# Kernel tuning notes

Measured on AMD Instinct MI355X. Metric: run time of the kernel, lower is better.

Reference implementation:

```python
import jax, jax.numpy as jnp
import numpy as np

K = 4  # number of conv kernel experts in CondConv_down


def setup_inputs() -> dict:
    key = jax.random.key(0)
    ks = jax.random.split(key, 8)
    N, Cin, H, W = 8, 64, 384, 384
    Cin2, Cout4, Cout2 = Cin // 2, 128 // 4, 128 // 2  # 32, 32, 64
    return {
        "x": jax.random.normal(ks[0], (N, Cin, H, W), jnp.float32),
        # square conv: Conv2d(in=64, out=64, 3x3, stride 2, pad 1, bias)
        "sq_w": jax.random.normal(ks[1], (Cout2, Cin, 3, 3), jnp.float32) * 0.05,
        "sq_b": jnp.zeros((Cout2,), jnp.float32),
        # vertical CondConv: attention 1x1 conv (== linear on pooled feats) + K expert kernels [3,1]
        "att_w_v": jax.random.normal(ks[2], (K, Cin2), jnp.float32) * 0.1,
        "att_b_v": jnp.zeros((K,), jnp.float32),
        "w_v": jax.random.normal(ks[3], (K, Cout4, Cin2, 3, 1), jnp.float32) * 0.05,
        "bn_v_g": jnp.ones((Cout4,), jnp.float32),
        "bn_v_b": jnp.zeros((Cout4,), jnp.float32),
        # horizontal CondConv: K expert kernels [1,3]
        "att_w_h": jax.random.normal(ks[4], (K, Cin2), jnp.float32) * 0.1,
        "att_b_h": jnp.zeros((K,), jnp.float32),
        "w_h": jax.random.normal(ks[5], (K, Cout4, Cin2, 1, 3), jnp.float32) * 0.05,
        "bn_h_g": jnp.ones((Cout4,), jnp.float32),
        "bn_h_b": jnp.zeros((Cout4,), jnp.float32),
    }


def _condconv(x, att_w, att_b, w, pad):
    # Attention: global avg pool -> 1x1 conv -> sigmoid (note: sigmoid, not softmax, as in source)
    att = jax.nn.sigmoid(jnp.mean(x, axis=(2, 3)) @ att_w.T + att_b)  # [N, K]
    # Aggregate expert kernels per sample: [N, Cout, Cin, kh, kw]
    agg = jnp.einsum("nk,koihw->noihw", att, w)
    def one(xi, wi):
        return jax.lax.conv_general_dilated(
            xi[None], wi, window_strides=(2, 2),
            padding=[(pad[0], pad[0]), (pad[1], pad[1])],
            dimension_numbers=("NCHW", "OIHW", "NCHW"))[0]
    return jax.vmap(one)(x, agg)  # per-sample dynamic conv == groups=N grouped conv


def _bn(x, g, b, eps=1e-5):
    # training-mode BatchNorm2d: batch statistics over (N, H, W), biased variance
    m = jnp.mean(x, axis=(0, 2, 3), keepdims=True)
    v = jnp.var(x, axis=(0, 2, 3), keepdims=True)
    return (x - m) * jax.lax.rsqrt(v + eps) * g[None, :, None, None] + b[None, :, None, None]


def _shuffle(x, g=8):
    N, C, H, W = x.shape
    return x.reshape(N, g, C // g, H, W).transpose(0, 2, 1, 3, 4).reshape(N, C, H, W)


def reference(x, sq_w, sq_b, att_w_v, att_b_v, w_v, bn_v_g, bn_v_b,
              att_w_h, att_b_h, w_h, bn_h_g, bn_h_b):
    sq = jax.lax.conv_general_dilated(
        x, sq_w, window_strides=(2, 2), padding=[(1, 1), (1, 1)],
        dimension_numbers=("NCHW", "OIHW", "NCHW")) + sq_b[None, :, None, None]
    x1, x2 = jnp.split(x, 2, axis=1)
    v = _bn(_condconv(x1, att_w_v, att_b_v, w_v, (1, 0)), bn_v_g, bn_v_b)
    h = _bn(_condconv(x2, att_w_h, att_b_h, w_h, (0, 1)), bn_h_g, bn_h_b)
    out = jnp.concatenate([sq, v, h], axis=1)  # [N, 128, H/2, W/2]
    return _shuffle(out, 8)
```

## Files before the change

kernel.cpp:

```cpp
#include <hip/hip_runtime.h>

#define NB    8
#define HIN   384
#define WIN   384
#define HOUT  192
#define WOUT  192
#define HW_IN (HIN * WIN)
#define PLANE (HOUT * WOUT)
#define CNT_BN (NB * HOUT * WOUT)

#define WS_MEANS 0
#define WS_AGGV  512
#define WS_AGGH  25088
#define WS_SQW   49664
#define WS_STATS 86528
#define WS_BN    86656

__global__ void k_zero(float* __restrict__ ws) {
    for (int i = threadIdx.x; i < 512; i += 256) ws[WS_MEANS + i] = 0.f;
    if (threadIdx.x < 128) ws[WS_STATS + threadIdx.x] = 0.f;
}

__global__ __launch_bounds__(256) void k_means(const float* __restrict__ x,
                                               float* __restrict__ ws) {
    int bc = blockIdx.x;
    int part = blockIdx.y;
    const float4* p = (const float4*)(x + (size_t)bc * HW_IN) + part * (HW_IN / 16);
    float s = 0.f;
    for (int i = threadIdx.x; i < HW_IN / 16; i += 256) {
        float4 v = p[i];
        s += (v.x + v.y) + (v.z + v.w);
    }
    __shared__ float red[256];
    red[threadIdx.x] = s;
    __syncthreads();
    for (int off = 128; off > 0; off >>= 1) {
        if ((int)threadIdx.x < off) red[threadIdx.x] += red[threadIdx.x + off];
        __syncthreads();
    }
    if (threadIdx.x == 0) atomicAdd(&ws[WS_MEANS + bc], red[0]);
}

__global__ void k_agg(const float* __restrict__ aw_v, const float* __restrict__ ab_v,
                      const float* __restrict__ wv,
                      const float* __restrict__ aw_h, const float* __restrict__ ab_h,
                      const float* __restrict__ wh, float* __restrict__ ws) {
    int n = blockIdx.x;
    __shared__ float att[8];
    if (threadIdx.x < 8) {
        int k = threadIdx.x & 3;
        int hsel = threadIdx.x >> 2;
        const float* m = ws + WS_MEANS + n * 64 + hsel * 32;
        const float* aw = hsel ? aw_h : aw_v;
        const float* ab = hsel ? ab_h : ab_v;
        float dot = 0.f;
        for (int c = 0; c < 32; c++) dot += m[c] * aw[k * 32 + c];
        float z = ab[k] + dot * (1.0f / HW_IN);
        att[threadIdx.x] = 1.0f / (1.0f + expf(-z));
    }
    __syncthreads();
    for (int i = threadIdx.x; i < 3072; i += 256) {
        int o = i & 31;
        int r = i >> 5;
        float sv = 0.f, sh = 0.f;
#pragma unroll
        for (int k = 0; k < 4; k++) {
            sv += att[k]     * wv[(k * 32 + o) * 96 + r];
            sh += att[4 + k] * wh[(k * 32 + o) * 96 + r];
        }
        ws[WS_AGGV + n * 3072 + i] = sv;
        ws[WS_AGGH + n * 3072 + i] = sh;
    }
}

__global__ void k_cvtw(const float* __restrict__ sq_w, float* __restrict__ ws) {
    int i = blockIdx.x * 256 + threadIdx.x;
    int oc = i & 63;
    int r = i >> 6;
    int c = r / 9, q = r % 9;
    ws[WS_SQW + i] = sq_w[(oc * 64 + c) * 9 + q];
}

__global__ __launch_bounds__(192) void k_sq(const float* __restrict__ x,
                                            const float* __restrict__ sq_b,
                                            const float* __restrict__ ws,
                                            float* __restrict__ out) {
    int xo = threadIdx.x;
    int yo = blockIdx.x;
    int n  = blockIdx.y;
    const float* wp = ws + WS_SQW;
    float acc[64];
#pragma unroll
    for (int j = 0; j < 64; j++) acc[j] = sq_b[j];
    const float* xb = x + (size_t)n * 64 * HW_IN;
    int c2 = 2 * xo;
    int iy0 = 2 * yo - 1;
    for (int c = 0; c < 64; c++) {
        const float* xc = xb + (size_t)c * HW_IN;
        float v[9];
#pragma unroll
        for (int ky = 0; ky < 3; ky++) {
            int iy = iy0 + ky;
            if (iy >= 0) {
                const float* row = xc + (size_t)iy * WIN;
                float2 v12 = *(const float2*)(row + c2);
                v[ky * 3 + 0] = (xo > 0) ? row[c2 - 1] : 0.f;
                v[ky * 3 + 1] = v12.x;
                v[ky * 3 + 2] = v12.y;
            } else {
                v[ky * 3 + 0] = v[ky * 3 + 1] = v[ky * 3 + 2] = 0.f;
            }
        }
        const float* wc = wp + c * 576;
#pragma unroll
        for (int t = 0; t < 9; t++) {
            float vv = v[t];
#pragma unroll
            for (int j = 0; j < 64; j++) acc[j] += vv * wc[t * 64 + j];
        }
    }
    size_t ob = (size_t)n * 128 * PLANE + (size_t)yo * WOUT + xo;
#pragma unroll
    for (int j = 0; j < 64; j++) {
        int co = ((j & 15) << 3) | (j >> 4);
        out[ob + (size_t)co * PLANE] = acc[j];
    }
}

__global__ __launch_bounds__(192) void k_vh(const float* __restrict__ x,
                                            const float* __restrict__ ws,
                                            float* __restrict__ out) {
    int xo = threadIdx.x, yo = blockIdx.x, n = blockIdx.y;
    int horz = blockIdx.z;
    float acc[32];
#pragma unroll
    for (int j = 0; j < 32; j++) acc[j] = 0.f;
    if (!horz) {
        const float* wn = ws + WS_AGGV + n * 3072;
        const float* xb = x + (size_t)n * 64 * HW_IN;
        int c2 = 2 * xo;
        int iy0 = 2 * yo - 1;
#pragma unroll 4
        for (int c = 0; c < 32; c++) {
            const float* xc = xb + (size_t)c * HW_IN;
            float v[3];
#pragma unroll
            for (int t = 0; t < 3; t++) {
                int iy = iy0 + t;
                v[t] = (iy >= 0) ? xc[(size_t)iy * WIN + c2] : 0.f;
            }
#pragma unroll
            for (int t = 0; t < 3; t++) {
                const float* wr = wn + (c * 3 + t) * 32;
#pragma unroll
                for (int j = 0; j < 32; j++) acc[j] += v[t] * wr[j];
            }
        }
    } else {
        const float* wn = ws + WS_AGGH + n * 3072;
        const float* xb = x + ((size_t)n * 64 + 32) * HW_IN;
        int c2 = 2 * xo;
#pragma unroll 4
        for (int c = 0; c < 32; c++) {
            const float* row = xb + (size_t)c * HW_IN + (size_t)(2 * yo) * WIN;
            float2 v12 = *(const float2*)(row + c2);
            float v0 = (xo > 0) ? row[c2 - 1] : 0.f;
            const float* wr = wn + c * 96;
#pragma unroll
            for (int j = 0; j < 32; j++)
                acc[j] += v0 * wr[j] + v12.x * wr[32 + j] + v12.y * wr[64 + j];
        }
    }
    int cb = horz ? 96 : 64;
    size_t ob = (size_t)n * 128 * PLANE + (size_t)yo * WOUT + xo;
#pragma unroll
    for (int j = 0; j < 32; j++) {
        int ci = cb + j;
        int co = ((ci & 15) << 3) | (ci >> 4);
        out[ob + (size_t)co * PLANE] = acc[j];
    }
}

__global__ __launch_bounds__(256) void k_stats(const float* __restrict__ out,
                                               float* __restrict__ ws) {
    int sch = blockIdx.x;
    int n = blockIdx.y;
    int vh = sch >> 5, oc = sch & 31;
    int ci = 64 + sch;
    int co = ((ci & 15) << 3) | (ci >> 4);
    const float4* p = (const float4*)(out + (size_t)(n * 128 + co) * PLANE);
    float s = 0.f, q = 0.f;
    for (int i = threadIdx.x; i < PLANE / 4; i += 256) {
        float4 v = p[i];
        s += (v.x + v.y) + (v.z + v.w);
        q += (v.x * v.x + v.y * v.y) + (v.z * v.z + v.w * v.w);
    }
    __shared__ float rs[256], rq[256];
    rs[threadIdx.x] = s; rq[threadIdx.x] = q;
    __syncthreads();
    for (int off = 128; off > 0; off >>= 1) {
        if ((int)threadIdx.x < off) {
            rs[threadIdx.x] += rs[threadIdx.x + off];
            rq[threadIdx.x] += rq[threadIdx.x + off];
        }
        __syncthreads();
    }
    if (threadIdx.x == 0) {
        atomicAdd(&ws[WS_STATS + vh * 64 + oc], rs[0]);
        atomicAdd(&ws[WS_STATS + vh * 64 + 32 + oc], rq[0]);
    }
}

__global__ void k_bnfin(const float* __restrict__ gv, const float* __restrict__ bv,
                        const float* __restrict__ gh, const float* __restrict__ bh,
                        float* __restrict__ ws) {
    int t = threadIdx.x;
    if (t >= 64) return;
    int vh = t >> 5;
    int c = t & 31;
    const float* st = ws + WS_STATS + vh * 64;
    float mean = st[c] * (1.0f / CNT_BN);
    float var = st[32 + c] * (1.0f / CNT_BN) - mean * mean;
    float g = vh ? gh[c] : gv[c];
    float b = vh ? bh[c] : bv[c];
    float scale = g * rsqrtf(var + 1e-5f);
    float* bn = ws + WS_BN + vh * 64;
    bn[c] = scale;
    bn[32 + c] = b - mean * scale;
}

__global__ __launch_bounds__(256) void k_apply(float* __restrict__ out,
                                               const float* __restrict__ ws) {
    int sch = blockIdx.x;
    int n = blockIdx.y;
    int vh = sch >> 5, oc = sch & 31;
    int ci = 64 + sch;
    int co = ((ci & 15) << 3) | (ci >> 4);
    const float* bn = ws + WS_BN + vh * 64;
    float scale = bn[oc], shift = bn[32 + oc];
    float4* p = (float4*)(out + (size_t)(n * 128 + co) * PLANE);
    for (int i = threadIdx.x; i < PLANE / 4; i += 256) {
        float4 v = p[i];
        v.x = v.x * scale + shift;
        v.y = v.y * scale + shift;
        v.z = v.z * scale + shift;
        v.w = v.w * scale + shift;
        p[i] = v;
    }
}

extern "C" void kernel_launch(void* const* d_in, const int* in_sizes, int n_in,
                              void* d_out, int out_size, void* d_ws, size_t ws_size,
                              hipStream_t stream) {
    const float* x    = (const float*)d_in[0];
    const float* sq_w = (const float*)d_in[1];
    const float* sq_b = (const float*)d_in[2];
    const float* aw_v = (const float*)d_in[3];
    const float* ab_v = (const float*)d_in[4];
    const float* w_v  = (const float*)d_in[5];
    const float* gv   = (const float*)d_in[6];
    const float* bv   = (const float*)d_in[7];
    const float* aw_h = (const float*)d_in[8];
    const float* ab_h = (const float*)d_in[9];
    const float* w_h  = (const float*)d_in[10];
    const float* gh   = (const float*)d_in[11];
    const float* bh   = (const float*)d_in[12];
    float* out = (float*)d_out;
    float* ws = (float*)d_ws;

    hipLaunchKernelGGL(k_zero, dim3(1), dim3(256), 0, stream, ws);
    hipLaunchKernelGGL(k_means, dim3(512, 4), dim3(256), 0, stream, x, ws);
    hipLaunchKernelGGL(k_agg, dim3(8), dim3(256), 0, stream,
                       aw_v, ab_v, w_v, aw_h, ab_h, w_h, ws);
    hipLaunchKernelGGL(k_cvtw, dim3(144), dim3(256), 0, stream, sq_w, ws);
    hipLaunchKernelGGL(k_vh, dim3(192, 8, 2), dim3(192), 0, stream, x, ws, out);
    hipLaunchKernelGGL(k_stats, dim3(64, 8), dim3(256), 0, stream, out, ws);
    hipLaunchKernelGGL(k_bnfin, dim3(1), dim3(64), 0, stream, gv, bv, gh, bh, ws);
    hipLaunchKernelGGL(k_apply, dim3(64, 8), dim3(256), 0, stream, out, ws);
    hipLaunchKernelGGL(k_sq, dim3(192, 8), dim3(192), 0, stream, x, sq_b, ws, out);
}
```

Baseline: 999.0 us.

## Compute two output columns per thread in conv kernels with float4 loads

The square, vertical and horizontal conv kernels now have each thread compute two adjacent output pixels. Each thread reads a float4 of input plus one left-neighbour value, so every weight load feeds two accumulators and the overlapping input column is shared. Each thread then writes a float2 per channel. Blocks now cover two output rows, which halves the grid. The combined vert/horz kernel is split into two separate launches to remove the branch. Doubling the accumulators (128 registers in k_sq) raises register pressure and may reduce occupancy or cause spills.

Measured after the change: 2.537 ms. +153.9%, slower.

```diff
diff --git a/kernel.cpp b/kernel.cpp
--- a/kernel.cpp
+++ b/kernel.cpp
@@ -85,99 +85,135 @@
                                             const float* __restrict__ sq_b,
                                             const float* __restrict__ ws,
                                             float* __restrict__ out) {
-    int xo = threadIdx.x;
-    int yo = blockIdx.x;
+    int tid = threadIdx.x;
+    int i = tid % 96;
+    int r = tid / 96;
+    int yo = blockIdx.x * 2 + r;
     int n  = blockIdx.y;
     const float* wp = ws + WS_SQW;
-    float acc[64];
-#pragma unroll
-    for (int j = 0; j < 64; j++) acc[j] = sq_b[j];
+    float acc0[64], acc1[64];
+#pragma unroll
+    for (int j = 0; j < 64; j++) { acc0[j] = sq_b[j]; acc1[j] = acc0[j]; }
     const float* xb = x + (size_t)n * 64 * HW_IN;
-    int c2 = 2 * xo;
+    int c4 = 4 * i;
     int iy0 = 2 * yo - 1;
     for (int c = 0; c < 64; c++) {
         const float* xc = xb + (size_t)c * HW_IN;
-        float v[9];
+        float4 vv[3];
+        float sm[3];
 #pragma unroll
         for (int ky = 0; ky < 3; ky++) {
             int iy = iy0 + ky;
+            const float* row = xc + (size_t)iy * WIN + c4;
             if (iy >= 0) {
-                const float* row = xc + (size_t)iy * WIN;
-                float2 v12 = *(const float2*)(row + c2);
-                v[ky * 3 + 0] = (xo > 0) ? row[c2 - 1] : 0.f;
-                v[ky * 3 + 1] = v12.x;
-                v[ky * 3 + 2] = v12.y;
+                vv[ky] = *(const float4*)row;
+                sm[ky] = (i > 0) ? row[-1] : 0.f;
             } else {
-                v[ky * 3 + 0] = v[ky * 3 + 1] = v[ky * 3 + 2] = 0.f;
+                vv[ky] = make_float4(0.f, 0.f, 0.f, 0.f);
+                sm[ky] = 0.f;
             }
         }
         const float* wc = wp + c * 576;
 #pragma unroll
-        for (int t = 0; t < 9; t++) {
-            float vv = v[t];
-#pragma unroll
-            for (int j = 0; j < 64; j++) acc[j] += vv * wc[t * 64 + j];
-        }
-    }
-    size_t ob = (size_t)n * 128 * PLANE + (size_t)yo * WOUT + xo;
+        for (int ky = 0; ky < 3; ky++) {
+            const float* w0 = wc + ky * 192;
+            float s = sm[ky];
+            float4 v = vv[ky];
+#pragma unroll
+            for (int j = 0; j < 64; j++) {
+                float wa = w0[j], wb = w0[64 + j], wcv = w0[128 + j];
+                acc0[j] += s   * wa + v.x * wb + v.y * wcv;
+                acc1[j] += v.y * wa + v.z * wb + v.w * wcv;
+            }
+        }
+    }
+    size_t ob = (size_t)n * 128 * PLANE + (size_t)yo * WOUT + 2 * i;
 #pragma unroll
     for (int j = 0; j < 64; j++) {
         int co = ((j & 15) << 3) | (j >> 4);
-        out[ob + (size_t)co * PLANE] = acc[j];
-    }
-}
-
-__global__ __launch_bounds__(192) void k_vh(const float* __restrict__ x,
-                                            const float* __restrict__ ws,
-                                            float* __restrict__ out) {
-    int xo = threadIdx.x, yo = blockIdx.x, n = blockIdx.y;
-    int horz = blockIdx.z;
-    float acc[32];
-#pragma unroll
-    for (int j = 0; j < 32; j++) acc[j] = 0.f;
-    if (!horz) {
-        const float* wn = ws + WS_AGGV + n * 3072;
-        const float* xb = x + (size_t)n * 64 * HW_IN;
-        int c2 = 2 * xo;
-        int iy0 = 2 * yo - 1;
-#pragma unroll 4
-        for (int c = 0; c < 32; c++) {
-            const float* xc = xb + (size_t)c * HW_IN;
-            float v[3];
-#pragma unroll
-            for (int t = 0; t < 3; t++) {
-                int iy = iy0 + t;
-                v[t] = (iy >= 0) ? xc[(size_t)iy * WIN + c2] : 0.f;
+        *(float2*)(out + ob + (size_t)co * PLANE) = make_float2(acc0[j], acc1[j]);
+    }
+}
+
+__global__ __launch_bounds__(192) void k_vert(const float* __restrict__ x,
+                                              const float* __restrict__ ws,
+                                              float* __restrict__ out) {
+    int tid = threadIdx.x;
+    int i = tid % 96;
+    int r = tid / 96;
+    int yo = blockIdx.x * 2 + r;
+    int n  = blockIdx.y;
+    const float* wn = ws + WS_AGGV + n * 3072;
+    float acc0[32], acc1[32];
+#pragma unroll
+    for (int j = 0; j < 32; j++) { acc0[j] = 0.f; acc1[j] = 0.f; }
+    const float* xb = x + (size_t)n * 64 * HW_IN;
+    int c4 = 4 * i;
+    int iy0 = 2 * yo - 1;
+#pragma unroll 2
+    for (int c = 0; c < 32; c++) {
+        const float* xc = xb + (size_t)c * HW_IN;
+        float4 vv[3];
+#pragma unroll
+        for (int t = 0; t < 3; t++) {
+            int iy = iy0 + t;
+            const float* row = xc + (size_t)iy * WIN + c4;
+            vv[t] = (iy >= 0) ? *(const float4*)row : make_float4(0.f, 0.f, 0.f, 0.f);
+        }
+#pragma unroll
+        for (int t = 0; t < 3; t++) {
+            const float* wr = wn + (c * 3 + t) * 32;
+            float va = vv[t].x, vb = vv[t].z;
+#pragma unroll
+            for (int j = 0; j < 32; j++) {
+                float w = wr[j];
+                acc0[j] += va * w;
+                acc1[j] += vb * w;
             }
-#pragma unroll
-            for (int t = 0; t < 3; t++) {
-                const float* wr = wn + (c * 3 + t) * 32;
-#pragma unroll
-                for (int j = 0; j < 32; j++) acc[j] += v[t] * wr[j];
-            }
-        }
-    } else {
-        const float* wn = ws + WS_AGGH + n * 3072;
-        const float* xb = x + ((size_t)n * 64 + 32) * HW_IN;
-        int c2 = 2 * xo;
-#pragma unroll 4
-        for (int c = 0; c < 32; c++) {
-            const float* row = xb + (size_t)c * HW_IN + (size_t)(2 * yo) * WIN;
-            float2 v12 = *(const float2*)(row + c2);
-            float v0 = (xo > 0) ? row[c2 - 1] : 0.f;
-            const float* wr = wn + c * 96;
-#pragma unroll
-            for (int j = 0; j < 32; j++)
-                acc[j] += v0 * wr[j] + v12.x * wr[32 + j] + v12.y * wr[64 + j];
-        }
-    }
-    int cb = horz ? 96 : 64;
-    size_t ob = (size_t)n * 128 * PLANE + (size_t)yo * WOUT + xo;
+        }
+    }
+    size_t ob = (size_t)n * 128 * PLANE + (size_t)yo * WOUT + 2 * i;
 #pragma unroll
     for (int j = 0; j < 32; j++) {
-        int ci = cb + j;
+        int ci = 64 + j;
         int co = ((ci & 15) << 3) | (ci >> 4);
-        out[ob + (size_t)co * PLANE] = acc[j];
+        *(float2*)(out + ob + (size_t)co * PLANE) = make_float2(acc0[j], acc1[j]);
+    }
+}
+
+__global__ __launch_bounds__(192) void k_horz(const float* __restrict__ x,
+                                              const float* __restrict__ ws,
+                                              float* __restrict__ out) {
+    int tid = threadIdx.x;
+    int i = tid % 96;
+    int r = tid / 96;
+    int yo = blockIdx.x * 2 + r;
+    int n  = blockIdx.y;
+    const float* wn = ws + WS_AGGH + n * 3072;
+    float acc0[32], acc1[32];
+#pragma unroll
+    for (int j = 0; j < 32; j++) { acc0[j] = 0.f; acc1[j] = 0.f; }
+    const float* xb = x + ((size_t)n * 64 + 32) * HW_IN;
+    int c4 = 4 * i;
+#pragma unroll 2
+    for (int c = 0; c < 32; c++) {
+        const float* row = xb + (size_t)c * HW_IN + (size_t)(2 * yo) * WIN + c4;
+        float4 v = *(const float4*)row;
+        float vm1 = (i > 0) ? row[-1] : 0.f;
+        const float* wr = wn + c * 96;
+#pragma unroll
+        for (int j = 0; j < 32; j++) {
+            float w0 = wr[j], w1 = wr[32 + j], w2 = wr[64 + j];
+            acc0[j] += vm1 * w0 + v.x * w1 + v.y * w2;
+            acc1[j] += v.y * w0 + v.z * w1 + v.w * w2;
+        }
+    }
+    size_t ob = (size_t)n * 128 * PLANE + (size_t)yo * WOUT + 2 * i;
+#pragma unroll
+    for (int j = 0; j < 32; j++) {
+        int ci = 96 + j;
+        int co = ((ci & 15) << 3) | (ci >> 4);
+        *(float2*)(out + ob + (size_t)co * PLANE) = make_float2(acc0[j], acc1[j]);
     }
 }
 
@@ -273,9 +309,10 @@
     hipLaunchKernelGGL(k_agg, dim3(8), dim3(256), 0, stream,
                        aw_v, ab_v, w_v, aw_h, ab_h, w_h, ws);
     hipLaunchKernelGGL(k_cvtw, dim3(144), dim3(256), 0, stream, sq_w, ws);
-    hipLaunchKernelGGL(k_vh, dim3(192, 8, 2), dim3(192), 0, stream, x, ws, out);
+    hipLaunchKernelGGL(k_vert, dim3(96, 8), dim3(192), 0, stream, x, ws, out);
+    hipLaunchKernelGGL(k_horz, dim3(96, 8), dim3(192), 0, stream, x, ws, out);
     hipLaunchKernelGGL(k_stats, dim3(64, 8), dim3(256), 0, stream, out, ws);
     hipLaunchKernelGGL(k_bnfin, dim3(1), dim3(64), 0, stream, gv, bv, gh, bh, ws);
     hipLaunchKernelGGL(k_apply, dim3(64, 8), dim3(256), 0, stream, out, ws);
-    hipLaunchKernelGGL(k_sq, dim3(192, 8), dim3(192), 0, stream, x, sq_b, ws, out);
-}
+    hipLaunchKernelGGL(k_sq, dim3(96, 8), dim3(192), 0, stream, x, sq_b, ws, out);
+}
```
